# Optimization experiments

Hardware: AMD Instinct MI355X
Metric: run time of the kernel (lower is better)

The kernel has to match this reference:

```python
import jax, jax.numpy as jnp
import numpy as np

HEADS = 8
DIM_HEAD = 32
SCALE = DIM_HEAD ** -0.5
EPS = 1e-5


def _layernorm_gamma(x, gamma):
    # GammaLayerNorm: zero-mean/unit-var over last dim, learnable gamma, no bias
    mu = jnp.mean(x, axis=-1, keepdims=True)
    var = jnp.var(x, axis=-1, keepdims=True)
    return (x - mu) * jax.lax.rsqrt(var + EPS) * gamma


def setup_inputs() -> dict:
    key = jax.random.key(0)
    k1, k2, k3 = jax.random.split(key, 3)
    B, N, D = 8, 16384, 256
    hidden = HEADS * DIM_HEAD  # 256
    x = jax.random.normal(k1, (B, N, D), dtype=jnp.float32)
    Wqkv = jax.random.normal(k2, (D, 3 * hidden), dtype=jnp.float32) * (D ** -0.5)
    Wout = jax.random.normal(k3, (hidden, D), dtype=jnp.float32) * (hidden ** -0.5)
    gamma = jnp.ones((D,), dtype=jnp.float32)
    return {"x": x, "Wqkv": Wqkv, "Wout": Wout, "gamma": gamma}


def reference(x, Wqkv, Wout, gamma):
    B, N, D = x.shape
    qkv = x @ Wqkv  # [B, N, 3*hidden]
    q, k, v = jnp.split(qkv, 3, axis=-1)

    def to_heads(t):  # b n (h d) -> b h n d
        return t.reshape(B, N, HEADS, DIM_HEAD).transpose(0, 2, 1, 3)

    q, k, v = map(to_heads, (q, k, v))
    q = jax.nn.softmax(q, axis=-1) * SCALE  # softmax over feature dim d
    k = jax.nn.softmax(k, axis=2)           # softmax over token dim n
    context = jnp.einsum('bhnd,bhne->bhde', k, v)  # [B,H,d,e] small kv state
    out = jnp.einsum('bhde,bhnd->bhne', context, q)  # [B,H,N,e]
    out = out.transpose(0, 2, 1, 3).reshape(B, N, HEADS * DIM_HEAD)
    out = out @ Wout
    return _layernorm_gamma(out, gamma)
```

## Files before the change

### kernel.cpp

```cpp
#include <hip/hip_runtime.h>
#include <hip/hip_bf16.h>

typedef __attribute__((ext_vector_type(8))) short short8;
typedef __attribute__((ext_vector_type(4))) float f32x4;

constexpr int SEQ = 16384, BATCH = 8, DIN = 256, NQKV = 768;
constexpr float SCALE = 0.17677669529663687f;
constexpr float EPS = 1e-5f;

__device__ __forceinline__ unsigned short f2bf(float f){
  __hip_bfloat16 h = __float2bfloat16(f);
  unsigned short u; __builtin_memcpy(&u, &h, 2); return u;
}
__device__ __forceinline__ float bf2f(unsigned short h){
  return __uint_as_float(((unsigned int)h) << 16);
}
__device__ __forceinline__ void gload_lds16(const void* g, void* l){
  __builtin_amdgcn_global_load_lds(
    (const __attribute__((address_space(1))) unsigned int*)g,
    (__attribute__((address_space(3))) unsigned int*)l, 16, 0, 0);
}
__device__ __forceinline__ void lds_barrier(){
  asm volatile("s_waitcnt lgkmcnt(0)" ::: "memory");
  __builtin_amdgcn_s_barrier();
}

__global__ void k_wt(const float* __restrict__ W, unsigned short* __restrict__ WT){
  int id = blockIdx.x * 256 + threadIdx.x;
  int k = id / NQKV, n = id % NQKV;
  WT[n * DIN + k] = f2bf(W[id]);
}

__global__ __launch_bounds__(256) void k_qkv(const float* __restrict__ X,
                                             const unsigned short* __restrict__ WT,
                                             unsigned short* __restrict__ Q,
                                             float* __restrict__ ctxp,
                                             float* __restrict__ sumwp){
  __shared__ unsigned short Bs[2][32 * 256];
  __shared__ unsigned short WVs[2][32][136];
  __shared__ float sumLds[256];
  const int blk = blockIdx.x;
  const size_t m0 = (size_t)blk * 128;
  const int tid = threadIdx.x, wave = tid >> 6, lane = tid & 63;
  const int lg = lane >> 4, li = lane & 15;
  sumLds[tid] = 0.f;
  unsigned short* qs = &WVs[0][0][0];

  auto panelN0 = [](int p){
    return (p < 16) ? (((p & 1) ? 512 : 256) + (p >> 1) * 32) : (p - 16) * 32;
  };
  auto stageB = [&](int buf, int n0){
    #pragma unroll
    for (int it = 0; it < 4; it++){
      int L = (it * 256 + tid) * 16;
      int G = L ^ (((L >> 9) & 7) << 4);
      gload_lds16((const char*)WT + (size_t)(n0 + (L >> 9)) * 512 + (G & 511),
                  (char*)Bs[buf] + L);
    }
  };

  stageB(0, panelN0(0));
  short8 afrag[2][8];
  #pragma unroll
  for (int rt = 0; rt < 2; rt++){
    const float* xr = X + (m0 + wave * 32 + rt * 16 + li) * 256 + lg * 8;
    #pragma unroll
    for (int ks = 0; ks < 8; ks++){
      float4 f0 = *reinterpret_cast<const float4*>(xr + ks * 32);
      float4 f1 = *reinterpret_cast<const float4*>(xr + ks * 32 + 4);
      short8 a;
      a[0] = f2bf(f0.x); a[1] = f2bf(f0.y); a[2] = f2bf(f0.z); a[3] = f2bf(f0.w);
      a[4] = f2bf(f1.x); a[5] = f2bf(f1.y); a[6] = f2bf(f1.z); a[7] = f2bf(f1.w);
      afrag[rt][ks] = a;
    }
  }
  #pragma unroll
  for (int rt = 0; rt < 2; rt++)
    #pragma unroll
    for (int ks = 0; ks < 8; ks++)
      asm volatile("" : "+v"(afrag[rt][ks]));
  __syncthreads();

  const f32x4 zf = {0.f, 0.f, 0.f, 0.f};
  int buf = 0;
  #pragma unroll 1
  for (int p = 0; p < 24; ++p){
    if (p < 23) stageB(buf ^ 1, panelN0(p + 1));
    f32x4 acc[2][2];
    acc[0][0] = zf; acc[0][1] = zf; acc[1][0] = zf; acc[1][1] = zf;
    __builtin_amdgcn_s_setprio(1);
    #pragma unroll
    for (int ks = 0; ks < 8; ks++)
      #pragma unroll
      for (int j = 0; j < 2; j++){
        int nl = j * 16 + li;
        int L = nl * 512 + (ks * 32 + lg * 8) * 2;
        short8 bb = *reinterpret_cast<const short8*>((const char*)Bs[buf] + (L ^ ((nl & 7) << 4)));
        acc[0][j] = __builtin_amdgcn_mfma_f32_16x16x32_bf16(afrag[0][ks], bb, acc[0][j], 0, 0, 0);
        acc[1][j] = __builtin_amdgcn_mfma_f32_16x16x32_bf16(afrag[1][ks], bb, acc[1][j], 0, 0, 0);
      }
    __builtin_amdgcn_s_setprio(0);
    if (p < 16){
      int h = p >> 1;
      if (!(p & 1)){
        #pragma unroll
        for (int j = 0; j < 2; j++){
          float cs = 0.f;
          #pragma unroll
          for (int rt = 0; rt < 2; rt++){
            unsigned short h0 = f2bf(__expf(acc[rt][j][0]));
            unsigned short h1 = f2bf(__expf(acc[rt][j][1]));
            unsigned short h2 = f2bf(__expf(acc[rt][j][2]));
            unsigned short h3 = f2bf(__expf(acc[rt][j][3]));
            cs += bf2f(h0) + bf2f(h1) + bf2f(h2) + bf2f(h3);
            ushort4 pk; pk.x = h0; pk.y = h1; pk.z = h2; pk.w = h3;
            *reinterpret_cast<ushort4*>(&WVs[0][j * 16 + li][wave * 32 + rt * 16 + lg * 4]) = pk;
          }
          cs += __shfl_xor(cs, 16); cs += __shfl_xor(cs, 32);
          if (lane < 16) atomicAdd(&sumLds[h * 32 + j * 16 + li], cs);
        }
      } else {
        #pragma unroll
        for (int j = 0; j < 2; j++)
          #pragma unroll
          for (int rt = 0; rt < 2; rt++){
            ushort4 pk;
            pk.x = f2bf(acc[rt][j][0]); pk.y = f2bf(acc[rt][j][1]);
            pk.z = f2bf(acc[rt][j][2]); pk.w = f2bf(acc[rt][j][3]);
            *reinterpret_cast<ushort4*>(&WVs[1][j * 16 + li][wave * 32 + rt * 16 + lg * 4]) = pk;
          }
      }
      __syncthreads();
      if (p & 1){
        int dh = wave >> 1, eh = wave & 1;
        f32x4 c = zf;
        #pragma unroll
        for (int ks = 0; ks < 4; ks++){
          short8 aw = *reinterpret_cast<const short8*>(&WVs[0][dh * 16 + li][ks * 32 + lg * 8]);
          short8 bv = *reinterpret_cast<const short8*>(&WVs[1][eh * 16 + li][ks * 32 + lg * 8]);
          c = __builtin_amdgcn_mfma_f32_16x16x32_bf16(aw, bv, c, 0, 0, 0);
        }
        float* cp = ctxp + ((size_t)blk * 8 + h) * 1024;
        #pragma unroll
        for (int r = 0; r < 4; r++)
          cp[(dh * 16 + lg * 4 + r) * 32 + eh * 16 + li] = c[r];
        lds_barrier();
      }
    } else {
      int ph = p - 16;
      #pragma unroll
      for (int rt = 0; rt < 2; rt++)
        #pragma unroll
        for (int j = 0; j < 2; j++)
          #pragma unroll
          for (int r = 0; r < 4; r++)
            qs[(wave * 32 + rt * 16 + lg * 4 + r) * 40 + j * 16 + li]
              = f2bf(acc[rt][j][r]);
      lds_barrier();
      {
        int row = tid >> 2, c8 = (tid & 3) * 8;
        #pragma unroll
        for (int rr = 0; rr < 2; rr++){
          short8 v = *reinterpret_cast<const short8*>(&qs[(rr * 64 + row) * 40 + c8]);
          *reinterpret_cast<short8*>(&Q[(m0 + rr * 64 + row) * 256 + ph * 32 + c8]) = v;
        }
      }
      __syncthreads();
    }
    buf ^= 1;
  }
  sumwp[(size_t)blk * 256 + tid] = sumLds[tid];
}

__global__ __launch_bounds__(256) void k_red1(const float* __restrict__ ctxp,
                                              const float* __restrict__ sumwp,
                                              float* __restrict__ ctxr,
                                              float* __restrict__ sumr){
  int bid = blockIdx.x;
  int s = bid & 15, bh = bid >> 4;
  int b = bh >> 3, h = bh & 7;
  int t = threadIdx.x;
  float a[4] = {0.f, 0.f, 0.f, 0.f};
  #pragma unroll
  for (int k = 0; k < 8; k++){
    const float* cp = ctxp + ((size_t)(b * 128 + s * 8 + k) * 8 + h) * 1024;
    #pragma unroll
    for (int q = 0; q < 4; q++) a[q] += cp[q * 256 + t];
  }
  float* orow = ctxr + (size_t)bid * 1024;
  #pragma unroll
  for (int q = 0; q < 4; q++) orow[q * 256 + t] = a[q];
  if (t < 32){
    float sw = 0.f;
    #pragma unroll
    for (int k = 0; k < 8; k++)
      sw += sumwp[(size_t)(b * 128 + s * 8 + k) * 256 + h * 32 + t];
    sumr[(size_t)bid * 32 + t] = sw;
  }
}

__global__ __launch_bounds__(256) void k_build_m(const float* __restrict__ ctxr,
                                                 const float* __restrict__ sumr,
                                                 const float* __restrict__ Wout,
                                                 unsigned short* __restrict__ MT){
  __shared__ float ctxs[32][33];
  __shared__ float swb[32];
  int b = blockIdx.x >> 3, h = blockIdx.x & 7;
  int bh16 = (b * 8 + h) * 16;
  int t = threadIdx.x;
  int e = t & 31, dq = t >> 5;
  float a0 = 0.f, a1 = 0.f, a2 = 0.f, a3 = 0.f;
  #pragma unroll
  for (int s = 0; s < 16; s++){
    const float* cp = ctxr + (size_t)(bh16 + s) * 1024;
    a0 += cp[dq * 32 + e];         a1 += cp[(dq + 8) * 32 + e];
    a2 += cp[(dq + 16) * 32 + e];  a3 += cp[(dq + 24) * 32 + e];
  }
  if (t < 32){
    float sw = 0.f;
    #pragma unroll
    for (int s = 0; s < 16; s++) sw += sumr[(size_t)(bh16 + s) * 32 + t];
    swb[t] = sw;
  }
  __syncthreads();
  ctxs[dq][e]      = a0 / swb[dq];
  ctxs[dq + 8][e]  = a1 / swb[dq + 8];
  ctxs[dq + 16][e] = a2 / swb[dq + 16];
  ctxs[dq + 24][e] = a3 / swb[dq + 24];
  __syncthreads();
  float s[32];
  #pragma unroll
  for (int d = 0; d < 32; d++) s[d] = 0.f;
  for (int ee = 0; ee < 32; ee++){
    float wv = Wout[(size_t)(h * 32 + ee) * 256 + t];
    #pragma unroll
    for (int d = 0; d < 32; d++) s[d] += ctxs[d][ee] * wv;
  }
  unsigned short* mp = MT + (size_t)b * 65536 + (size_t)t * 256 + h * 32;
  #pragma unroll
  for (int d8 = 0; d8 < 4; d8++){
    short8 pk;
    #pragma unroll
    for (int q = 0; q < 8; q++) pk[q] = (short)f2bf(s[d8 * 8 + q]);
    *reinterpret_cast<short8*>(mp + d8 * 8) = pk;
  }
}

__global__ __launch_bounds__(256, 4) void k_out(const unsigned short* __restrict__ Qm,
                                                const unsigned short* __restrict__ MT,
                                                const float* __restrict__ gamma,
                                                float* __restrict__ out){
  __shared__ unsigned short Bs[64 * 256];
  const int blk = blockIdx.x;
  const int b = blk >> 8;
  const size_t m0 = (size_t)blk * 64;
  const int tid = threadIdx.x, wave = tid >> 6, lane = tid & 63;
  const int lg = lane >> 4, li = lane & 15;

  short8 afrag[8];
  {
    const unsigned short* qr = Qm + (m0 + wave * 16 + li) * 256 + lg * 8;
    #pragma unroll
    for (int ks = 0; ks < 8; ks++)
      afrag[ks] = *reinterpret_cast<const short8*>(qr + ks * 32);
  }
  #pragma unroll
  for (int ks = 0; ks < 8; ks++){
    float v[8];
    #pragma unroll
    for (int q = 0; q < 8; q++) v[q] = bf2f((unsigned short)afrag[ks][q]);
    float mx = v[0];
    #pragma unroll
    for (int q = 1; q < 8; q++) mx = fmaxf(mx, v[q]);
    mx = fmaxf(mx, __shfl_xor(mx, 16));
    mx = fmaxf(mx, __shfl_xor(mx, 32));
    float s = 0.f;
    #pragma unroll
    for (int q = 0; q < 8; q++){ v[q] = __expf(v[q] - mx); s += v[q]; }
    s += __shfl_xor(s, 16);
    s += __shfl_xor(s, 32);
    float iv = SCALE / s;
    #pragma unroll
    for (int q = 0; q < 8; q++) afrag[ks][q] = (short)f2bf(v[q] * iv);
  }

  const char* mtb = (const char*)MT + (size_t)b * 131072;
  f32x4 acc[4][4];
  const f32x4 zf = {0.f, 0.f, 0.f, 0.f};
  #pragma unroll
  for (int jb = 0; jb < 4; jb++)
    #pragma unroll
    for (int j = 0; j < 4; j++) acc[jb][j] = zf;

  #pragma unroll
  for (int jb = 0; jb < 4; jb++){
    if (jb) __syncthreads();
    #pragma unroll
    for (int rr = 0; rr < 8; rr++){
      int L = rr * 4096 + tid * 16;
      int G = L ^ (((L >> 9) & 7) << 4);
      gload_lds16(mtb + (size_t)jb * 32768 + G, (char*)Bs + L);
    }
    __syncthreads();
    #pragma unroll
    for (int ks = 0; ks < 8; ks++)
      #pragma unroll
      for (int j = 0; j < 4; j++){
        int n = j * 16 + li;
        int L = n * 512 + (ks * 32 + lg * 8) * 2;
        short8 bb = *reinterpret_cast<const short8*>((const char*)Bs + (L ^ ((n & 7) << 4)));
        acc[jb][j] = __builtin_amdgcn_mfma_f32_16x16x32_bf16(afrag[ks], bb, acc[jb][j], 0, 0, 0);
      }
  }

  float gam[16];
  #pragma unroll
  for (int jb = 0; jb < 4; jb++)
    #pragma unroll
    for (int j = 0; j < 4; j++) gam[jb * 4 + j] = gamma[jb * 64 + j * 16 + li];
  #pragma unroll
  for (int r = 0; r < 4; r++){
    float s = 0.f, qq = 0.f;
    #pragma unroll
    for (int jb = 0; jb < 4; jb++)
      #pragma unroll
      for (int j = 0; j < 4; j++){ float v = acc[jb][j][r]; s += v; qq += v * v; }
    #pragma unroll
    for (int mm = 1; mm < 16; mm <<= 1){ s += __shfl_xor(s, mm); qq += __shfl_xor(qq, mm); }
    float mu = s * (1.f / 256.f);
    float var = qq * (1.f / 256.f) - mu * mu;
    float inv = rsqrtf(var + EPS);
    float* op = out + (m0 + wave * 16 + lg * 4 + r) * 256;
    #pragma unroll
    for (int jb = 0; jb < 4; jb++)
      #pragma unroll
      for (int j = 0; j < 4; j++)
        op[jb * 64 + j * 16 + li] = (acc[jb][j][r] - mu) * inv * gam[jb * 4 + j];
  }
}

extern "C" void kernel_launch(void* const* d_in, const int* in_sizes, int n_in,
                              void* d_out, int out_size, void* d_ws, size_t ws_size,
                              hipStream_t stream){
  const float* x     = (const float*)d_in[0];
  const float* Wqkv  = (const float*)d_in[1];
  const float* Wout  = (const float*)d_in[2];
  const float* gamma = (const float*)d_in[3];
  float* out = (float*)d_out;

  char* ws = (char*)d_ws;
  size_t off = 0;
  unsigned short* Q   = (unsigned short*)(ws + off); off += (size_t)BATCH * SEQ * 256 * 2;
  unsigned short* WT  = (unsigned short*)(ws + off); off += (size_t)NQKV * DIN * 2;
  float* ctxp         = (float*)(ws + off);          off += (size_t)1024 * 8 * 1024 * 4;
  float* sumwp        = (float*)(ws + off);          off += (size_t)1024 * 256 * 4;
  float* ctxr         = (float*)(ws + off);          off += (size_t)1024 * 1024 * 4;
  float* sumr         = (float*)(ws + off);          off += (size_t)1024 * 32 * 4;
  unsigned short* MT  = (unsigned short*)(ws + off); off += (size_t)BATCH * 65536 * 2;

  k_wt<<<(NQKV * DIN) / 256, 256, 0, stream>>>(Wqkv, WT);
  k_qkv<<<1024, 256, 0, stream>>>(x, WT, Q, ctxp, sumwp);
  k_red1<<<1024, 256, 0, stream>>>(ctxp, sumwp, ctxr, sumr);
  k_build_m<<<64, 256, 0, stream>>>(ctxr, sumr, Wout, MT);
  k_out<<<2048, 256, 0, stream>>>(Q, MT, gamma, out);
}
```

Measured before the change: 179.0 us.

## Double QKV block rows and replace partial-context reduction kernel with atomics

The QKV kernel now handles 256 rows per 512-thread block, and its per-block context and sum partials are accumulated with global atomicAdd into a per-batch buffer that is zeroed by a memset. This removes the separate k_red1 reduction kernel and its large partial-buffer round trip, and k_build_m now reads the reduced context directly. In exchange it adds atomic contention on 64 small tiles, a larger LDS footprint, and fewer blocks in flight. Floating-point summation order also becomes nondeterministic. The hidden middle section of the kernel must also fit the new 512-thread layout.

```diff
diff --git a/kernel.cpp b/kernel.cpp
--- a/kernel.cpp
+++ b/kernel.cpp
@@ -31,19 +31,20 @@
   WT[n * DIN + k] = f2bf(W[id]);
 }
 
-__global__ __launch_bounds__(256) void k_qkv(const float* __restrict__ X,
-                                             const unsigned short* __restrict__ WT,
-                                             unsigned short* __restrict__ Q,
-                                             float* __restrict__ ctxp,
-                                             float* __restrict__ sumwp){
+__global__ __launch_bounds__(512, 4) void k_qkv(const float* __restrict__ X,
+                                                const unsigned short* __restrict__ WT,
+                                                unsigned short* __restrict__ Q,
+                                                float* __restrict__ ctxg,
+                                                float* __restrict__ sumg){
   __shared__ unsigned short Bs[2][32 * 256];
-  __shared__ unsigned short WVs[2][32][136];
+  __shared__ unsigned short WVs[2][32][264];
   __shared__ float sumLds[256];
   const int blk = blockIdx.x;
-  const size_t m0 = (size_t)blk * 128;
+  const size_t m0 = (size_t)blk * 256;
+  const int b = blk >> 6;
   const int tid = threadIdx.x, wave = tid >> 6, lane = tid & 63;
   const int lg = lane >> 4, li = lane & 15;
-  sumLds[tid] = 0.f;
+  if (tid < 256) sumLds[tid] = 0.f;
   unsigned short* qs = &WVs[0][0][0];
 
   auto panelN0 = [](int p){
@@ -51,8 +52,8 @@
   };
   auto stageB = [&](int buf, int n0){
     #pragma unroll
-    for (int it = 0; it < 4; it++){
-      int L = (it * 256 + tid) * 16;
+    for (int it = 0; it < 2; it++){
+      int L = (it * 512 + tid) * 16;
       int G = L ^ (((L >> 9) & 7) << 4);
       gload_lds16((const char*)WT + (size_t)(n0 + (L >> 9)) * 512 + (G & 511),
                   (char*)Bs[buf] + L);
@@ -132,18 +133,18 @@
       }
       __syncthreads();
       if (p & 1){
-        int dh = wave >> 1, eh = wave & 1;
+        int th = wave >> 2, dh = (wave >> 1) & 1, eh = wave & 1;
         f32x4 c = zf;
         #pragma unroll
         for (int ks = 0; ks < 4; ks++){
-          short8 aw = *reinterpret_cast<const short8*>(&WVs[0][dh * 16 + li][ks * 32 + lg * 8]);
-          short8 bv = *reinterpret_cast<const short8*>(&WVs[1][eh * 16 + li][ks * 32 + lg * 8]);
+          short8 aw = *reinterpret_cast<const short8*>(&WVs[0][dh * 16 + li][th * 128 + ks * 32 + lg * 8]);
+          short8 bv = *reinterpret_cast<const short8*>(&WVs[1][eh * 16 + li][th * 128 + ks * 32 + lg * 8]);
           c = __builtin_amdgcn_mfma_f32_16x16x32_bf16(aw, bv, c, 0, 0, 0);
         }
-        float* cp = ctxp + ((size_t)blk * 8 + h) * 1024;
+        float* cp = ctxg + ((size_t)(b * 8 + h)) * 1024;
         #pragma unroll
         for (int r = 0; r < 4; r++)
-          cp[(dh * 16 + lg * 4 + r) * 32 + eh * 16 + li] = c[r];
+          atomicAdd(&cp[(dh * 16 + lg * 4 + r) * 32 + eh * 16 + li], c[r]);
         lds_barrier();
       }
     } else {
@@ -161,72 +162,33 @@
         int row = tid >> 2, c8 = (tid & 3) * 8;
         #pragma unroll
         for (int rr = 0; rr < 2; rr++){
-          short8 v = *reinterpret_cast<const short8*>(&qs[(rr * 64 + row) * 40 + c8]);
-          *reinterpret_cast<short8*>(&Q[(m0 + rr * 64 + row) * 256 + ph * 32 + c8]) = v;
+          short8 v = *reinterpret_cast<const short8*>(&qs[(rr * 128 + row) * 40 + c8]);
+          *reinterpret_cast<short8*>(&Q[(m0 + rr * 128 + row) * 256 + ph * 32 + c8]) = v;
         }
       }
       __syncthreads();
     }
     buf ^= 1;
   }
-  sumwp[(size_t)blk * 256 + tid] = sumLds[tid];
-}
-
-__global__ __launch_bounds__(256) void k_red1(const float* __restrict__ ctxp,
-                                              const float* __restrict__ sumwp,
-                                              float* __restrict__ ctxr,
-                                              float* __restrict__ sumr){
-  int bid = blockIdx.x;
-  int s = bid & 15, bh = bid >> 4;
-  int b = bh >> 3, h = bh & 7;
-  int t = threadIdx.x;
-  float a[4] = {0.f, 0.f, 0.f, 0.f};
-  #pragma unroll
-  for (int k = 0; k < 8; k++){
-    const float* cp = ctxp + ((size_t)(b * 128 + s * 8 + k) * 8 + h) * 1024;
-    #pragma unroll
-    for (int q = 0; q < 4; q++) a[q] += cp[q * 256 + t];
-  }
-  float* orow = ctxr + (size_t)bid * 1024;
-  #pragma unroll
-  for (int q = 0; q < 4; q++) orow[q * 256 + t] = a[q];
-  if (t < 32){
-    float sw = 0.f;
-    #pragma unroll
-    for (int k = 0; k < 8; k++)
-      sw += sumwp[(size_t)(b * 128 + s * 8 + k) * 256 + h * 32 + t];
-    sumr[(size_t)bid * 32 + t] = sw;
-  }
-}
-
-__global__ __launch_bounds__(256) void k_build_m(const float* __restrict__ ctxr,
-                                                 const float* __restrict__ sumr,
+  if (tid < 256) atomicAdd(&sumg[b * 256 + tid], sumLds[tid]);
+}
+
+__global__ __launch_bounds__(256) void k_build_m(const float* __restrict__ ctxg,
+                                                 const float* __restrict__ sumg,
                                                  const float* __restrict__ Wout,
                                                  unsigned short* __restrict__ MT){
   __shared__ float ctxs[32][33];
   __shared__ float swb[32];
   int b = blockIdx.x >> 3, h = blockIdx.x & 7;
-  int bh16 = (b * 8 + h) * 16;
   int t = threadIdx.x;
   int e = t & 31, dq = t >> 5;
-  float a0 = 0.f, a1 = 0.f, a2 = 0.f, a3 = 0.f;
-  #pragma unroll
-  for (int s = 0; s < 16; s++){
-    const float* cp = ctxr + (size_t)(bh16 + s) * 1024;
-    a0 += cp[dq * 32 + e];         a1 += cp[(dq + 8) * 32 + e];
-    a2 += cp[(dq + 16) * 32 + e];  a3 += cp[(dq + 24) * 32 + e];
-  }
-  if (t < 32){
-    float sw = 0.f;
-    #pragma unroll
-    for (int s = 0; s < 16; s++) sw += sumr[(size_t)(bh16 + s) * 32 + t];
-    swb[t] = sw;
-  }
+  const float* cg = ctxg + (size_t)blockIdx.x * 1024;
+  if (t < 32) swb[t] = sumg[b * 256 + h * 32 + t];
   __syncthreads();
-  ctxs[dq][e]      = a0 / swb[dq];
-  ctxs[dq + 8][e]  = a1 / swb[dq + 8];
-  ctxs[dq + 16][e] = a2 / swb[dq + 16];
-  ctxs[dq + 24][e] = a3 / swb[dq + 24];
+  ctxs[dq][e]      = cg[dq * 32 + e]        / swb[dq];
+  ctxs[dq + 8][e]  = cg[(dq + 8) * 32 + e]  / swb[dq + 8];
+  ctxs[dq + 16][e] = cg[(dq + 16) * 32 + e] / swb[dq + 16];
+  ctxs[dq + 24][e] = cg[(dq + 24) * 32 + e] / swb[dq + 24];
   __syncthreads();
   float s[32];
   #pragma unroll
@@ -352,15 +314,13 @@
   size_t off = 0;
   unsigned short* Q   = (unsigned short*)(ws + off); off += (size_t)BATCH * SEQ * 256 * 2;
   unsigned short* WT  = (unsigned short*)(ws + off); off += (size_t)NQKV * DIN * 2;
-  float* ctxp         = (float*)(ws + off);          off += (size_t)1024 * 8 * 1024 * 4;
-  float* sumwp        = (float*)(ws + off);          off += (size_t)1024 * 256 * 4;
-  float* ctxr         = (float*)(ws + off);          off += (size_t)1024 * 1024 * 4;
-  float* sumr         = (float*)(ws + off);          off += (size_t)1024 * 32 * 4;
+  float* ctxg         = (float*)(ws + off);          off += (size_t)64 * 1024 * 4;
+  float* sumg         = (float*)(ws + off);          off += (size_t)BATCH * 256 * 4;
   unsigned short* MT  = (unsigned short*)(ws + off); off += (size_t)BATCH * 65536 * 2;
 
   k_wt<<<(NQKV * DIN) / 256, 256, 0, stream>>>(Wqkv, WT);
-  k_qkv<<<1024, 256, 0, stream>>>(x, WT, Q, ctxp, sumwp);
-  k_red1<<<1024, 256, 0, stream>>>(ctxp, sumwp, ctxr, sumr);
-  k_build_m<<<64, 256, 0, stream>>>(ctxr, sumr, Wout, MT);
+  hipMemsetAsync(ctxg, 0, (size_t)64 * 1024 * 4 + (size_t)BATCH * 256 * 4, stream);
+  k_qkv<<<512, 512, 0, stream>>>(x, WT, Q, ctxg, sumg);
+  k_build_m<<<64, 256, 0, stream>>>(ctxg, sumg, Wout, MT);
   k_out<<<2048, 256, 0, stream>>>(Q, MT, gamma, out);
 }
```

Result: slower. 190.7 us (+6.6%).

## Prefetch weight panels through registers with single LDS buffer and merged barriers

Applied to the files above, without the earlier changes.

Replaces the double-buffered direct global-to-LDS weight staging with a register prefetch: the next panel is loaded into registers while the current one is computed, then written into a single LDS buffer after a barrier. The per-panel epilogues (context MFMA for k/v panels, Q store for q panels) are moved after that barrier so each iteration uses one __syncthreads plus one lds_barrier instead of up to three barriers. This halves the weight LDS footprint, which may allow higher occupancy, but adds register pressure for the prefetch and makes the LDS write synchronous with the loop.

```diff
diff --git a/kernel.cpp b/kernel.cpp
--- a/kernel.cpp
+++ b/kernel.cpp
@@ -36,7 +36,7 @@
                                              unsigned short* __restrict__ Q,
                                              float* __restrict__ ctxp,
                                              float* __restrict__ sumwp){
-  __shared__ unsigned short Bs[2][32 * 256];
+  __shared__ unsigned short Bs[32 * 256];
   __shared__ unsigned short WVs[2][32][136];
   __shared__ float sumLds[256];
   const int blk = blockIdx.x;
@@ -49,17 +49,24 @@
   auto panelN0 = [](int p){
     return (p < 16) ? (((p & 1) ? 512 : 256) + (p >> 1) * 32) : (p - 16) * 32;
   };
-  auto stageB = [&](int buf, int n0){
-    #pragma unroll
-    for (int it = 0; it < 4; it++){
-      int L = (it * 256 + tid) * 16;
-      int G = L ^ (((L >> 9) & 7) << 4);
-      gload_lds16((const char*)WT + (size_t)(n0 + (L >> 9)) * 512 + (G & 511),
-                  (char*)Bs[buf] + L);
-    }
+  int4 pf[4];
+  auto pfIssue = [&](int n0){
+    const char* src = (const char*)WT + (size_t)(n0 + (tid >> 3)) * 512 + (tid & 7) * 64;
+    #pragma unroll
+    for (int q = 0; q < 4; q++)
+      pf[q] = *reinterpret_cast<const int4*>(src + q * 16);
   };
-
-  stageB(0, panelN0(0));
+  auto pfWrite = [&](){
+    int row = tid >> 3;
+    int base = row * 512 + (tid & 7) * 64;
+    #pragma unroll
+    for (int q = 0; q < 4; q++){
+      int L = base + q * 16;
+      *reinterpret_cast<int4*>((char*)Bs + (L ^ ((row & 7) << 4))) = pf[q];
+    }
+  };
+
+  pfIssue(panelN0(0));
   short8 afrag[2][8];
   #pragma unroll
   for (int rt = 0; rt < 2; rt++){
@@ -79,13 +86,13 @@
     #pragma unroll
     for (int ks = 0; ks < 8; ks++)
       asm volatile("" : "+v"(afrag[rt][ks]));
+  pfWrite();
   __syncthreads();
 
   const f32x4 zf = {0.f, 0.f, 0.f, 0.f};
-  int buf = 0;
   #pragma unroll 1
   for (int p = 0; p < 24; ++p){
-    if (p < 23) stageB(buf ^ 1, panelN0(p + 1));
+    if (p < 23) pfIssue(panelN0(p + 1));
     f32x4 acc[2][2];
     acc[0][0] = zf; acc[0][1] = zf; acc[1][0] = zf; acc[1][1] = zf;
     __builtin_amdgcn_s_setprio(1);
@@ -95,7 +102,7 @@
       for (int j = 0; j < 2; j++){
         int nl = j * 16 + li;
         int L = nl * 512 + (ks * 32 + lg * 8) * 2;
-        short8 bb = *reinterpret_cast<const short8*>((const char*)Bs[buf] + (L ^ ((nl & 7) << 4)));
+        short8 bb = *reinterpret_cast<const short8*>((const char*)Bs + (L ^ ((nl & 7) << 4)));
         acc[0][j] = __builtin_amdgcn_mfma_f32_16x16x32_bf16(afrag[0][ks], bb, acc[0][j], 0, 0, 0);
         acc[1][j] = __builtin_amdgcn_mfma_f32_16x16x32_bf16(afrag[1][ks], bb, acc[1][j], 0, 0, 0);
       }
@@ -130,24 +137,7 @@
             *reinterpret_cast<ushort4*>(&WVs[1][j * 16 + li][wave * 32 + rt * 16 + lg * 4]) = pk;
           }
       }
-      __syncthreads();
-      if (p & 1){
-        int dh = wave >> 1, eh = wave & 1;
-        f32x4 c = zf;
-        #pragma unroll
-        for (int ks = 0; ks < 4; ks++){
-          short8 aw = *reinterpret_cast<const short8*>(&WVs[0][dh * 16 + li][ks * 32 + lg * 8]);
-          short8 bv = *reinterpret_cast<const short8*>(&WVs[1][eh * 16 + li][ks * 32 + lg * 8]);
-          c = __builtin_amdgcn_mfma_f32_16x16x32_bf16(aw, bv, c, 0, 0, 0);
-        }
-        float* cp = ctxp + ((size_t)blk * 8 + h) * 1024;
-        #pragma unroll
-        for (int r = 0; r < 4; r++)
-          cp[(dh * 16 + lg * 4 + r) * 32 + eh * 16 + li] = c[r];
-        lds_barrier();
-      }
     } else {
-      int ph = p - 16;
       #pragma unroll
       for (int rt = 0; rt < 2; rt++)
         #pragma unroll
@@ -156,18 +146,33 @@
           for (int r = 0; r < 4; r++)
             qs[(wave * 32 + rt * 16 + lg * 4 + r) * 40 + j * 16 + li]
               = f2bf(acc[rt][j][r]);
-      lds_barrier();
-      {
-        int row = tid >> 2, c8 = (tid & 3) * 8;
-        #pragma unroll
-        for (int rr = 0; rr < 2; rr++){
-          short8 v = *reinterpret_cast<const short8*>(&qs[(rr * 64 + row) * 40 + c8]);
-          *reinterpret_cast<short8*>(&Q[(m0 + rr * 64 + row) * 256 + ph * 32 + c8]) = v;
-        }
-      }
-      __syncthreads();
-    }
-    buf ^= 1;
+    }
+    __syncthreads();
+    if (p < 23) pfWrite();
+    if (p < 16 && (p & 1)){
+      int h = p >> 1;
+      int dh = wave >> 1, eh = wave & 1;
+      f32x4 c = zf;
+      #pragma unroll
+      for (int ks = 0; ks < 4; ks++){
+        short8 aw = *reinterpret_cast<const short8*>(&WVs[0][dh * 16 + li][ks * 32 + lg * 8]);
+        short8 bv = *reinterpret_cast<const short8*>(&WVs[1][eh * 16 + li][ks * 32 + lg * 8]);
+        c = __builtin_amdgcn_mfma_f32_16x16x32_bf16(aw, bv, c, 0, 0, 0);
+      }
+      float* cp = ctxp + ((size_t)blk * 8 + h) * 1024;
+      #pragma unroll
+      for (int r = 0; r < 4; r++)
+        cp[(dh * 16 + lg * 4 + r) * 32 + eh * 16 + li] = c[r];
+    } else if (p >= 16){
+      int ph = p - 16;
+      int row = tid >> 2, c8 = (tid & 3) * 8;
+      #pragma unroll
+      for (int rr = 0; rr < 2; rr++){
+        short8 v = *reinterpret_cast<const short8*>(&qs[(rr * 64 + row) * 40 + c8]);
+        *reinterpret_cast<short8*>(&Q[(m0 + rr * 64 + row) * 256 + ph * 32 + c8]) = v;
+      }
+    }
+    lds_barrier();
   }
   sumwp[(size_t)blk * 256 + tid] = sumLds[tid];
 }
```

Measured after the change: 233.4 us. +30.4%, slower.

## Recompute Q projection inside output kernel instead of materializing Q in memory

Applied to the files above, without the earlier changes.

Removes the Q panels from the QKV kernel and drops the bf16 Q workspace. The output kernel now reloads x, multiplies by the Q slice of the transposed weights, and applies the feature softmax before the context GEMM. This avoids writing and re-reading the Q tensor, in exchange for re-reading fp32 x and doing an extra GEMM per tile. The occupancy hint on the output kernel is also dropped.

```diff
diff --git a/kernel.cpp b/kernel.cpp
--- a/kernel.cpp
+++ b/kernel.cpp
@@ -33,7 +33,6 @@
 
 __global__ __launch_bounds__(256) void k_qkv(const float* __restrict__ X,
                                              const unsigned short* __restrict__ WT,
-                                             unsigned short* __restrict__ Q,
                                              float* __restrict__ ctxp,
                                              float* __restrict__ sumwp){
   __shared__ unsigned short Bs[2][32 * 256];
@@ -44,10 +43,9 @@
   const int tid = threadIdx.x, wave = tid >> 6, lane = tid & 63;
   const int lg = lane >> 4, li = lane & 15;
   sumLds[tid] = 0.f;
-  unsigned short* qs = &WVs[0][0][0];
 
   auto panelN0 = [](int p){
-    return (p < 16) ? (((p & 1) ? 512 : 256) + (p >> 1) * 32) : (p - 16) * 32;
+    return ((p & 1) ? 512 : 256) + (p >> 1) * 32;
   };
   auto stageB = [&](int buf, int n0){
     #pragma unroll
@@ -84,8 +82,8 @@
   const f32x4 zf = {0.f, 0.f, 0.f, 0.f};
   int buf = 0;
   #pragma unroll 1
-  for (int p = 0; p < 24; ++p){
-    if (p < 23) stageB(buf ^ 1, panelN0(p + 1));
+  for (int p = 0; p < 16; ++p){
+    if (p < 15) stageB(buf ^ 1, panelN0(p + 1));
     f32x4 acc[2][2];
     acc[0][0] = zf; acc[0][1] = zf; acc[1][0] = zf; acc[1][1] = zf;
     __builtin_amdgcn_s_setprio(1);
@@ -100,72 +98,50 @@
         acc[1][j] = __builtin_amdgcn_mfma_f32_16x16x32_bf16(afrag[1][ks], bb, acc[1][j], 0, 0, 0);
       }
     __builtin_amdgcn_s_setprio(0);
-    if (p < 16){
-      int h = p >> 1;
-      if (!(p & 1)){
+    int h = p >> 1;
+    if (!(p & 1)){
+      #pragma unroll
+      for (int j = 0; j < 2; j++){
+        float cs = 0.f;
         #pragma unroll
-        for (int j = 0; j < 2; j++){
-          float cs = 0.f;
-          #pragma unroll
-          for (int rt = 0; rt < 2; rt++){
-            unsigned short h0 = f2bf(__expf(acc[rt][j][0]));
-            unsigned short h1 = f2bf(__expf(acc[rt][j][1]));
-            unsigned short h2 = f2bf(__expf(acc[rt][j][2]));
-            unsigned short h3 = f2bf(__expf(acc[rt][j][3]));
-            cs += bf2f(h0) + bf2f(h1) + bf2f(h2) + bf2f(h3);
-            ushort4 pk; pk.x = h0; pk.y = h1; pk.z = h2; pk.w = h3;
-            *reinterpret_cast<ushort4*>(&WVs[0][j * 16 + li][wave * 32 + rt * 16 + lg * 4]) = pk;
-          }
-          cs += __shfl_xor(cs, 16); cs += __shfl_xor(cs, 32);
-          if (lane < 16) atomicAdd(&sumLds[h * 32 + j * 16 + li], cs);
+        for (int rt = 0; rt < 2; rt++){
+          unsigned short h0 = f2bf(__expf(acc[rt][j][0]));
+          unsigned short h1 = f2bf(__expf(acc[rt][j][1]));
+          unsigned short h2 = f2bf(__expf(acc[rt][j][2]));
+          unsigned short h3 = f2bf(__expf(acc[rt][j][3]));
+          cs += bf2f(h0) + bf2f(h1) + bf2f(h2) + bf2f(h3);
+          ushort4 pk; pk.x = h0; pk.y = h1; pk.z = h2; pk.w = h3;
+          *reinterpret_cast<ushort4*>(&WVs[0][j * 16 + li][wave * 32 + rt * 16 + lg * 4]) = pk;
         }
-      } else {
+        cs += __shfl_xor(cs, 16); cs += __shfl_xor(cs, 32);
+        if (lane < 16) atomicAdd(&sumLds[h * 32 + j * 16 + li], cs);
+      }
+    } else {
+      #pragma unroll
+      for (int j = 0; j < 2; j++)
         #pragma unroll
-        for (int j = 0; j < 2; j++)
-          #pragma unroll
-          for (int rt = 0; rt < 2; rt++){
-            ushort4 pk;
-            pk.x = f2bf(acc[rt][j][0]); pk.y = f2bf(acc[rt][j][1]);
-            pk.z = f2bf(acc[rt][j][2]); pk.w = f2bf(acc[rt][j][3]);
-            *reinterpret_cast<ushort4*>(&WVs[1][j * 16 + li][wave * 32 + rt * 16 + lg * 4]) = pk;
-          }
-      }
-      __syncthreads();
-      if (p & 1){
-        int dh = wave >> 1, eh = wave & 1;
-        f32x4 c = zf;
-        #pragma unroll
-        for (int ks = 0; ks < 4; ks++){
-          short8 aw = *reinterpret_cast<const short8*>(&WVs[0][dh * 16 + li][ks * 32 + lg * 8]);
-          short8 bv = *reinterpret_cast<const short8*>(&WVs[1][eh * 16 + li][ks * 32 + lg * 8]);
-          c = __builtin_amdgcn_mfma_f32_16x16x32_bf16(aw, bv, c, 0, 0, 0);
+        for (int rt = 0; rt < 2; rt++){
+          ushort4 pk;
+          pk.x = f2bf(acc[rt][j][0]); pk.y = f2bf(acc[rt][j][1]);
+          pk.z = f2bf(acc[rt][j][2]); pk.w = f2bf(acc[rt][j][3]);
+          *reinterpret_cast<ushort4*>(&WVs[1][j * 16 + li][wave * 32 + rt * 16 + lg * 4]) = pk;
         }
-        float* cp = ctxp + ((size_t)blk * 8 + h) * 1024;
-        #pragma unroll
-        for (int r = 0; r < 4; r++)
-          cp[(dh * 16 + lg * 4 + r) * 32 + eh * 16 + li] = c[r];
-        lds_barrier();
-      }
-    } else {
-      int ph = p - 16;
-      #pragma unroll
-      for (int rt = 0; rt < 2; rt++)
-        #pragma unroll
-        for (int j = 0; j < 2; j++)
-          #pragma unroll
-          for (int r = 0; r < 4; r++)
-            qs[(wave * 32 + rt * 16 + lg * 4 + r) * 40 + j * 16 + li]
-              = f2bf(acc[rt][j][r]);
+    }
+    __syncthreads();
+    if (p & 1){
+      int dh = wave >> 1, eh = wave & 1;
+      f32x4 c = zf;
+      #pragma unroll
+      for (int ks = 0; ks < 4; ks++){
+        short8 aw = *reinterpret_cast<const short8*>(&WVs[0][dh * 16 + li][ks * 32 + lg * 8]);
+        short8 bv = *reinterpret_cast<const short8*>(&WVs[1][eh * 16 + li][ks * 32 + lg * 8]);
+        c = __builtin_amdgcn_mfma_f32_16x16x32_bf16(aw, bv, c, 0, 0, 0);
+      }
+      float* cp = ctxp + ((size_t)blk * 8 + h) * 1024;
+      #pragma unroll
+      for (int r = 0; r < 4; r++)
+        cp[(dh * 16 + lg * 4 + r) * 32 + eh * 16 + li] = c[r];
       lds_barrier();
-      {
-        int row = tid >> 2, c8 = (tid & 3) * 8;
-        #pragma unroll
-        for (int rr = 0; rr < 2; rr++){
-          short8 v = *reinterpret_cast<const short8*>(&qs[(rr * 64 + row) * 40 + c8]);
-          *reinterpret_cast<short8*>(&Q[(m0 + rr * 64 + row) * 256 + ph * 32 + c8]) = v;
-        }
-      }
-      __syncthreads();
     }
     buf ^= 1;
   }
@@ -246,52 +222,104 @@
   }
 }
 
-__global__ __launch_bounds__(256, 4) void k_out(const unsigned short* __restrict__ Qm,
-                                                const unsigned short* __restrict__ MT,
-                                                const float* __restrict__ gamma,
-                                                float* __restrict__ out){
+__global__ __launch_bounds__(256) void k_out(const float* __restrict__ X,
+                                             const unsigned short* __restrict__ WT,
+                                             const unsigned short* __restrict__ MT,
+                                             const float* __restrict__ gamma,
+                                             float* __restrict__ out){
   __shared__ unsigned short Bs[64 * 256];
   const int blk = blockIdx.x;
   const int b = blk >> 8;
   const size_t m0 = (size_t)blk * 64;
   const int tid = threadIdx.x, wave = tid >> 6, lane = tid & 63;
   const int lg = lane >> 4, li = lane & 15;
+  const f32x4 zf = {0.f, 0.f, 0.f, 0.f};
 
   short8 afrag[8];
   {
-    const unsigned short* qr = Qm + (m0 + wave * 16 + li) * 256 + lg * 8;
+    const float* xr = X + (m0 + wave * 16 + li) * 256 + lg * 8;
+    #pragma unroll
+    for (int ks = 0; ks < 8; ks++){
+      float4 f0 = *reinterpret_cast<const float4*>(xr + ks * 32);
+      float4 f1 = *reinterpret_cast<const float4*>(xr + ks * 32 + 4);
+      short8 a;
+      a[0] = f2bf(f0.x); a[1] = f2bf(f0.y); a[2] = f2bf(f0.z); a[3] = f2bf(f0.w);
+      a[4] = f2bf(f1.x); a[5] = f2bf(f1.y); a[6] = f2bf(f1.z); a[7] = f2bf(f1.w);
+      afrag[ks] = a;
+    }
+  }
+
+  f32x4 acc[4][4];
+  #pragma unroll
+  for (int jb = 0; jb < 4; jb++)
+    #pragma unroll
+    for (int j = 0; j < 4; j++) acc[jb][j] = zf;
+
+  const char* wqb = (const char*)WT;
+  #pragma unroll
+  for (int jb = 0; jb < 4; jb++){
+    if (jb) __syncthreads();
+    #pragma unroll
+    for (int rr = 0; rr < 8; rr++){
+      int L = rr * 4096 + tid * 16;
+      int G = L ^ (((L >> 9) & 7) << 4);
+      gload_lds16(wqb + (size_t)jb * 32768 + G, (char*)Bs + L);
+    }
+    __syncthreads();
     #pragma unroll
     for (int ks = 0; ks < 8; ks++)
-      afrag[ks] = *reinterpret_cast<const short8*>(qr + ks * 32);
-  }
+      #pragma unroll
+      for (int j = 0; j < 4; j++){
+        int n = j * 16 + li;
+        int L = n * 512 + (ks * 32 + lg * 8) * 2;
+        short8 bb = *reinterpret_cast<const short8*>((const char*)Bs + (L ^ ((n & 7) << 4)));
+        acc[jb][j] = __builtin_amdgcn_mfma_f32_16x16x32_bf16(afrag[ks], bb, acc[jb][j], 0, 0, 0);
+      }
+  }
+  __syncthreads();
+
+  #pragma unroll
+  for (int r = 0; r < 4; r++){
+    int row = wave * 16 + lg * 4 + r;
+    #pragma unroll
+    for (int jb = 0; jb < 4; jb++){
+      float a0 = acc[jb][0][r], a1 = acc[jb][1][r];
+      float b0 = acc[jb][2][r], b1 = acc[jb][3][r];
+      float mA = fmaxf(a0, a1), mB = fmaxf(b0, b1);
+      #pragma unroll
+      for (int mm = 1; mm < 16; mm <<= 1){
+        mA = fmaxf(mA, __shfl_xor(mA, mm)); mB = fmaxf(mB, __shfl_xor(mB, mm));
+      }
+      float e0 = __expf(a0 - mA), e1 = __expf(a1 - mA);
+      float e2 = __expf(b0 - mB), e3 = __expf(b1 - mB);
+      float sA = e0 + e1, sB = e2 + e3;
+      #pragma unroll
+      for (int mm = 1; mm < 16; mm <<= 1){
+        sA += __shfl_xor(sA, mm); sB += __shfl_xor(sB, mm);
+      }
+      float iA = SCALE / sA, iB = SCALE / sB;
+      int Lb = row * 512;
+      int sw = (row & 7) << 4;
+      *reinterpret_cast<unsigned short*>((char*)Bs + ((Lb + (jb * 64 + li) * 2) ^ sw))      = f2bf(e0 * iA);
+      *reinterpret_cast<unsigned short*>((char*)Bs + ((Lb + (jb * 64 + 16 + li) * 2) ^ sw)) = f2bf(e1 * iA);
+      *reinterpret_cast<unsigned short*>((char*)Bs + ((Lb + (jb * 64 + 32 + li) * 2) ^ sw)) = f2bf(e2 * iB);
+      *reinterpret_cast<unsigned short*>((char*)Bs + ((Lb + (jb * 64 + 48 + li) * 2) ^ sw)) = f2bf(e3 * iB);
+    }
+  }
+  lds_barrier();
   #pragma unroll
   for (int ks = 0; ks < 8; ks++){
-    float v[8];
-    #pragma unroll
-    for (int q = 0; q < 8; q++) v[q] = bf2f((unsigned short)afrag[ks][q]);
-    float mx = v[0];
-    #pragma unroll
-    for (int q = 1; q < 8; q++) mx = fmaxf(mx, v[q]);
-    mx = fmaxf(mx, __shfl_xor(mx, 16));
-    mx = fmaxf(mx, __shfl_xor(mx, 32));
-    float s = 0.f;
-    #pragma unroll
-    for (int q = 0; q < 8; q++){ v[q] = __expf(v[q] - mx); s += v[q]; }
-    s += __shfl_xor(s, 16);
-    s += __shfl_xor(s, 32);
-    float iv = SCALE / s;
-    #pragma unroll
-    for (int q = 0; q < 8; q++) afrag[ks][q] = (short)f2bf(v[q] * iv);
-  }
-
+    int row = wave * 16 + li;
+    int L = row * 512 + (ks * 32 + lg * 8) * 2;
+    afrag[ks] = *reinterpret_cast<const short8*>((const char*)Bs + (L ^ ((row & 7) << 4)));
+  }
+  __syncthreads();
+
+  #pragma unroll
+  for (int jb = 0; jb < 4; jb++)
+    #pragma unroll
+    for (int j = 0; j < 4; j++) acc[jb][j] = zf;
   const char* mtb = (const char*)MT + (size_t)b * 131072;
-  f32x4 acc[4][4];
-  const f32x4 zf = {0.f, 0.f, 0.f, 0.f};
-  #pragma unroll
-  for (int jb = 0; jb < 4; jb++)
-    #pragma unroll
-    for (int j = 0; j < 4; j++) acc[jb][j] = zf;
-
   #pragma unroll
   for (int jb = 0; jb < 4; jb++){
     if (jb) __syncthreads();
@@ -350,8 +378,8 @@
 
   char* ws = (char*)d_ws;
   size_t off = 0;
-  unsigned short* Q   = (unsigned short*)(ws + off); off += (size_t)BATCH * SEQ * 256 * 2;
   unsigned short* WT  = (unsigned short*)(ws + off); off += (size_t)NQKV * DIN * 2;
+  off = (off + 255) & ~(size_t)255;
   float* ctxp         = (float*)(ws + off);          off += (size_t)1024 * 8 * 1024 * 4;
   float* sumwp        = (float*)(ws + off);          off += (size_t)1024 * 256 * 4;
   float* ctxr         = (float*)(ws + off);          off += (size_t)1024 * 1024 * 4;
@@ -359,8 +387,8 @@
   unsigned short* MT  = (unsigned short*)(ws + off); off += (size_t)BATCH * 65536 * 2;
 
   k_wt<<<(NQKV * DIN) / 256, 256, 0, stream>>>(Wqkv, WT);
-  k_qkv<<<1024, 256, 0, stream>>>(x, WT, Q, ctxp, sumwp);
+  k_qkv<<<1024, 256, 0, stream>>>(x, WT, ctxp, sumwp);
   k_red1<<<1024, 256, 0, stream>>>(ctxp, sumwp, ctxr, sumr);
   k_build_m<<<64, 256, 0, stream>>>(ctxr, sumr, Wout, MT);
-  k_out<<<2048, 256, 0, stream>>>(Q, MT, gamma, out);
-}
+  k_out<<<2048, 256, 0, stream>>>(x, WT, MT, gamma, out);
+}
```

After: 203.6 us. 13.8% more time.
